# Optimization experiments

Hardware: AMD Instinct MI355X
Metric: run time of the kernel (lower is better)

Reference implementation:

```python
import jax, jax.numpy as jnp
import numpy as np

N_NODES = 100000   # n_all_trajs
N_EDGES = 640000
HIDDEN = 128
N_USERS = 1000


def gcn_conv(x, edge_index, edge_weight, W, b, num_nodes):
    """PyG GCNConv with add_self_loops=False, normalize=True.
    out[col] += (deg^-1/2[row] * w * deg^-1/2[col]) * (x @ W)[row]; then + b.
    deg is weighted in-degree at the target (col) nodes."""
    row, col = edge_index[0], edge_index[1]
    deg = jax.ops.segment_sum(edge_weight, col, num_segments=num_nodes)
    deg_inv_sqrt = jnp.where(deg > 0, jax.lax.rsqrt(jnp.maximum(deg, 1e-30)), 0.0)
    norm = deg_inv_sqrt[row] * edge_weight * deg_inv_sqrt[col]   # [E]
    h = x @ W                                                    # [N, H]
    msg = h[row] * norm[:, None]                                 # [E, H] gather+scale
    out = jax.ops.segment_sum(msg, col, num_segments=num_nodes)  # scatter-add
    return out + b


def setup_inputs() -> dict:
    key = jax.random.key(0)
    ks = jax.random.split(key, 9)
    edge_index = jax.random.randint(ks[0], (2, N_EDGES), 0, N_NODES, dtype=jnp.int64)
    edge_weight = jax.random.uniform(ks[1], (N_EDGES,), dtype=jnp.float32)
    emb = jax.random.normal(ks[2], (N_NODES, HIDDEN), dtype=jnp.float32) * 0.02
    W1 = jax.random.normal(ks[3], (HIDDEN, HIDDEN), dtype=jnp.float32) * 0.05
    b1 = jax.random.normal(ks[4], (HIDDEN,), dtype=jnp.float32) * 0.01
    W2 = jax.random.normal(ks[5], (HIDDEN, HIDDEN), dtype=jnp.float32) * 0.05
    b2 = jax.random.normal(ks[6], (HIDDEN,), dtype=jnp.float32) * 0.01
    Wp = jax.random.normal(ks[7], (HIDDEN, N_USERS), dtype=jnp.float32) * 0.05
    bp = jax.random.normal(ks[8], (N_USERS,), dtype=jnp.float32) * 0.01
    return {"edge_index": edge_index, "edge_weight": edge_weight, "emb": emb,
            "W1": W1, "b1": b1, "W2": W2, "b2": b2, "Wp": Wp, "bp": bp}


def reference(edge_index, edge_weight, emb, W1, b1, W2, b2, Wp, bp):
    h1 = gcn_conv(emb, edge_index, edge_weight, W1, b1, N_NODES)
    # dropout p=0.0 (inference) -> identity
    h2 = gcn_conv(h1, edge_index, edge_weight, W2, b2, N_NODES)
    predictions = h2 @ Wp + bp   # [N_NODES, N_USERS]
    return predictions
```

## Files before the change

kernel.cpp:

```cpp
#include <hip/hip_runtime.h>

#define N_NODES 100000
#define N_EDGES 640000
#define HIDDEN  128
#define N_USERS 1000
#define CAP     64

using u16 = unsigned short;
using u32 = unsigned int;

using short8  = __attribute__((ext_vector_type(8))) short;
using floatx4 = __attribute__((ext_vector_type(4))) float;

__device__ __forceinline__ u16 f2bf(float f) {
  u32 u = __float_as_uint(f);
  u32 r = u + 0x7FFFu + ((u >> 16) & 1u);
  return (u16)(r >> 16);
}
__device__ __forceinline__ u32 pack2bf(float a, float b) {
  return (u32)f2bf(a) | ((u32)f2bf(b) << 16);
}
__device__ __forceinline__ float bflo2f(u32 v) { return __uint_as_float(v << 16); }


__global__ __launch_bounds__(256)
void prep_kernel(const float* __restrict__ emb, u16* __restrict__ xb,
                 const int* __restrict__ ecol, const float* __restrict__ ew,
                 float* __restrict__ deg,
                 const float* __restrict__ W1, const float* __restrict__ b1,
                 const float* __restrict__ W2,
                 float* __restrict__ T1, float* __restrict__ t1) {
  int b = blockIdx.x;
  if (b < 6250) {
    int i = b * 256 + threadIdx.x;
    const float4* s4 = (const float4*)(emb + (size_t)i * 8);
    float4 lo = s4[0], hi = s4[1];
    uint4 o;
    o.x = pack2bf(lo.x, lo.y); o.y = pack2bf(lo.z, lo.w);
    o.z = pack2bf(hi.x, hi.y); o.w = pack2bf(hi.z, hi.w);
    ((uint4*)xb)[i] = o;
  } else if (b < 8750) {
    int i = (b - 6250) * 256 + threadIdx.x;
    atomicAdd(&deg[ecol[i]], ew[i]);
  } else {
    int idx = (b - 8750) * 256 + threadIdx.x;
    if (idx >= 129 * 128) return;
    int k = idx >> 7, c = idx & 127;
    const float* src = (k < 128) ? (W1 + (size_t)k * 128) : b1;
    float s = 0.f;
    for (int j = 0; j < 128; ++j) s += src[j] * W2[(size_t)j * 128 + c];
    if (k < 128) T1[(size_t)k * 128 + c] = s;
    else         t1[c] = s;
  }
}

__global__ __launch_bounds__(256)
void stage2_kernel(const int* __restrict__ erow, const int* __restrict__ ecol,
                   const float* __restrict__ ew, const float* __restrict__ deg,
                   int* __restrict__ counts, int2* __restrict__ pairs,
                   const float* __restrict__ T1, const float* __restrict__ t1,
                   const float* __restrict__ b2, const float* __restrict__ Wp,
                   const float* __restrict__ bp,
                   u16* __restrict__ WcT, float* __restrict__ u, float* __restrict__ v) {
  int b = blockIdx.x;
  if (b < 2500) {
    int i = b * 256 + threadIdx.x;
    int r = erow[i], c = ecol[i];
    float dr = deg[r], dc = deg[c];
    float nr = dr > 0.f ? rsqrtf(dr) : 0.f;
    float nc = dc > 0.f ? rsqrtf(dc) : 0.f;
    int pos = atomicAdd(&counts[c], 1);
    if (pos < CAP)
      pairs[((size_t)c << 6) + (size_t)pos] = make_int2(r, __float_as_int(nr * ew[i] * nc));
  } else if (b < 3012) {
    int idx = (b - 2500) * 256 + threadIdx.x;
    int c = idx >> 7, k = idx & 127;
    float s = 0.f;
    if (c < N_USERS)
      for (int l = 0; l < 128; ++l) s += T1[(size_t)k * 128 + l] * Wp[(size_t)l * N_USERS + c];
    WcT[idx] = f2bf(s);
  } else {
    int idx = (b - 3012) * 256 + threadIdx.x;
    if (idx >= 2 * N_USERS) return;
    if (idx < N_USERS) {
      float s = 0.f;
      for (int j = 0; j < 128; ++j) s += t1[j] * Wp[(size_t)j * N_USERS + idx];
      u[idx] = s;
    } else {
      int c = idx - N_USERS;
      float s = bp[c];
      for (int j = 0; j < 128; ++j) s += b2[j] * Wp[(size_t)j * N_USERS + c];
      v[c] = s;
    }
  }
}

template<bool S1OUT>
__global__ __launch_bounds__(256)
void agg_kernel(const u16* __restrict__ hb, const int* __restrict__ counts,
                const int2* __restrict__ pairs, float* __restrict__ s1,
                u16* __restrict__ out, int M) {
  int wid  = threadIdx.x >> 6;
  int lane = threadIdx.x & 63;
  int n = blockIdx.x * 4 + wid;
  if (n >= M) return;
  int cnt = counts[n];
  cnt = cnt < CAP ? cnt : CAP;
  int2 my = make_int2(0, 0);
  if (lane < cnt) my = pairs[((size_t)n << 6) + lane];
  int   sv = my.x;
  float wv = __int_as_float(my.y);
  const uint2* h8 = (const uint2*)hb;
  int half = lane >> 5, l5 = lane & 31;
  float a0 = 0.f, a1 = 0.f, a2 = 0.f, a3 = 0.f;
  int trips = (cnt + 1) >> 1;
  int t = 0;
  for (; t + 2 <= trips; t += 2) {
    int e0 = 2 * t + half, e1 = 2 * t + 2 + half;
    int   s0 = __shfl(sv, e0), s1_ = __shfl(sv, e1);
    float w0 = __shfl(wv, e0), w1  = __shfl(wv, e1);
    uint2 h0 = h8[((size_t)s0  << 5) + l5];
    uint2 h1 = h8[((size_t)s1_ << 5) + l5];
    a0 += w0 * bflo2f(h0.x & 0xFFFFu); a1 += w0 * __uint_as_float(h0.x & 0xFFFF0000u);
    a2 += w0 * bflo2f(h0.y & 0xFFFFu); a3 += w0 * __uint_as_float(h0.y & 0xFFFF0000u);
    a0 += w1 * bflo2f(h1.x & 0xFFFFu); a1 += w1 * __uint_as_float(h1.x & 0xFFFF0000u);
    a2 += w1 * bflo2f(h1.y & 0xFFFFu); a3 += w1 * __uint_as_float(h1.y & 0xFFFF0000u);
  }
  for (; t < trips; ++t) {
    int e = 2 * t + half;
    int   s = __shfl(sv, e);
    float w = __shfl(wv, e);
    uint2 h = h8[((size_t)s << 5) + l5];
    a0 += w * bflo2f(h.x & 0xFFFFu); a1 += w * __uint_as_float(h.x & 0xFFFF0000u);
    a2 += w * bflo2f(h.y & 0xFFFFu); a3 += w * __uint_as_float(h.y & 0xFFFF0000u);
  }
  a0 += __shfl_xor(a0, 32); a1 += __shfl_xor(a1, 32);
  a2 += __shfl_xor(a2, 32); a3 += __shfl_xor(a3, 32);
  if (S1OUT) {
    float tt = wv;
    for (int o = 32; o; o >>= 1) tt += __shfl_xor(tt, o);
    if (lane == 0) s1[n] = tt;
  }
  if (half == 0) {
    uint2 o;
    o.x = pack2bf(a0, a1);
    o.y = pack2bf(a2, a3);
    ((uint2*)out)[((size_t)n << 5) + l5] = o;
  }
}

__global__ __launch_bounds__(256, 2)
void gemm_final(const u16* __restrict__ A, const u16* __restrict__ BT,
                const float* __restrict__ s1, const float* __restrict__ u,
                const float* __restrict__ vv, float* __restrict__ outf, int M) {
  __shared__ u16 smem[2 * 128 * 128];
  u16* As = smem;
  u16* Bs = smem + 128 * 128;
  const int m0 = (blockIdx.x >> 3) * 128;
  const int n0 = (blockIdx.x & 7) * 128;
  const int tid = threadIdx.x;

  for (int i = 0; i < 8; ++i) {
    int chunk = tid + i * 256;
    int row = chunk >> 4;
    int c   = chunk & 15;
    int sw  = ((c ^ (row & 15)) << 3);
    int gr  = m0 + row;
    uint4 av = {0u, 0u, 0u, 0u};
    if (gr < M) av = *(const uint4*)(A + ((size_t)gr << 7) + (c << 3));
    *(uint4*)(&As[(row << 7) + sw]) = av;
    uint4 bv = *(const uint4*)(BT + ((size_t)(n0 + row) << 7) + (c << 3));
    *(uint4*)(&Bs[(row << 7) + sw]) = bv;
  }
  __syncthreads();

  const int wid  = tid >> 6, lane = tid & 63;
  const int wr = (wid >> 1) << 6;
  const int wc = (wid & 1) << 6;
  const int lm = lane & 15, quad = lane >> 4;

  floatx4 acc[4][4] = {};
  for (int ks = 0; ks < 4; ++ks) {
    int cks = ks * 4 + quad;
    int sw  = ((cks ^ lm) << 3);
    short8 a[4], b[4];
    for (int i = 0; i < 4; ++i)
      a[i] = *(const short8*)(&As[((wr + i * 16 + lm) << 7) + sw]);
    for (int j = 0; j < 4; ++j)
      b[j] = *(const short8*)(&Bs[((wc + j * 16 + lm) << 7) + sw]);
    for (int i = 0; i < 4; ++i)
      for (int j = 0; j < 4; ++j)
        acc[i][j] = __builtin_amdgcn_mfma_f32_16x16x32_bf16(a[i], b[j], acc[i][j], 0, 0, 0);
  }

  float uc[4], vc[4];
  for (int j = 0; j < 4; ++j) {
    int col = n0 + wc + j * 16 + lm;
    bool ok = col < N_USERS;
    uc[j] = ok ? u[col]  : 0.f;
    vc[j] = ok ? vv[col] : 0.f;
  }
  float sr[4][4];
  for (int i = 0; i < 4; ++i)
    for (int r = 0; r < 4; ++r) {
      int row = m0 + wr + i * 16 + quad * 4 + r;
      sr[i][r] = (row < M) ? s1[row] : 0.f;
    }

  __syncthreads();
  float* Os = (float*)smem;
  for (int i = 0; i < 4; ++i)
    for (int j = 0; j < 4; ++j)
      for (int r = 0; r < 4; ++r) {
        int lrow = wr + i * 16 + quad * 4 + r;
        int lcol = wc + j * 16 + lm;
        Os[(lrow << 7) + lcol] = acc[i][j][r] + sr[i][r] * uc[j] + vc[j];
      }
  __syncthreads();

  for (int k = 0; k < 16; ++k) {
    int f   = k * 256 + tid;
    int row = f >> 5;
    int c4  = f & 31;
    int gr  = m0 + row;
    int col = n0 + (c4 << 2);
    if (gr < M && col < N_USERS) {
      float4 val = *(const float4*)(Os + (row << 7) + (c4 << 2));
      *(float4*)(outf + (size_t)gr * N_USERS + col) = val;
    }
  }
}

extern "C" void kernel_launch(void* const* d_in, const int* in_sizes, int n_in,
                              void* d_out, int out_size, void* d_ws, size_t ws_size,
                              hipStream_t stream) {
  const int*   eidx = (const int*)d_in[0];
  const int*   erow = eidx;
  const int*   ecol = eidx + N_EDGES;
  const float* ew   = (const float*)d_in[1];
  const float* emb  = (const float*)d_in[2];
  const float* W1   = (const float*)d_in[3];
  const float* b1   = (const float*)d_in[4];
  const float* W2   = (const float*)d_in[5];
  const float* b2   = (const float*)d_in[6];
  const float* Wp   = (const float*)d_in[7];
  const float* bp   = (const float*)d_in[8];
  float* out = (float*)d_out;

  const int M = N_NODES;

  char* p = (char*)d_ws;
  float* deg    = (float*)p;  p += 400128;
  int*   counts = (int*)p;    p += 400128;
  float* s1     = (float*)p;  p += 400128;
  int2*  pairs  = (int2*)p;   p += (size_t)M * CAP * 8;
  u16*   Xb     = (u16*)p;    p += (size_t)M * 128 * 2;
  u16*   g      = (u16*)p;    p += (size_t)M * 128 * 2;
  float* T1     = (float*)p;  p += 128 * 128 * 4;
  float* t1     = (float*)p;  p += 512;
  u16*   WcT    = (u16*)p;    p += 1024 * 128 * 2;
  float* uvec   = (float*)p;  p += 4096;
  float* vvec   = (float*)p;  p += 4096;

  hipMemsetAsync(deg, 0, 400128 + 400128, stream);

  prep_kernel<<<8815, 256, 0, stream>>>(emb, Xb, ecol, ew, deg, W1, b1, W2, T1, t1);
  stage2_kernel<<<3020, 256, 0, stream>>>(erow, ecol, ew, deg, counts, pairs,
                                          T1, t1, b2, Wp, bp, WcT, uvec, vvec);

  agg_kernel<true ><<<(M + 3) / 4, 256, 0, stream>>>(Xb, counts, pairs, s1, g, M);
  agg_kernel<false><<<(M + 3) / 4, 256, 0, stream>>>(g,  counts, pairs, nullptr, Xb, M);

  const int mt = (M + 127) / 128;
  gemm_final<<<mt * 8, 256, 0, stream>>>(Xb, WcT, s1, uvec, vvec, out, M);
}
```

Baseline: 699.4 us.

## Halve gemm_final LDS, read B from global, and group blocks for L2 reuse

The final GEMM no longer stages the B (WcT) tile in shared memory. B fragments are read straight from global memory, where the small 1000x128 matrix should stay in cache. The output staging is split into two 64-row halves so a single 32KB LDS buffer is enough, and launch bounds rise to 4 blocks per CU. Block indices are remapped so that 8 consecutive M tiles share the same N tile, which is meant to improve L2 locality. The trade-offs are uncoalesced global B loads inside the MFMA loop, extra barriers, and a hardcoded grid of 98*64 blocks tied to N_NODES.

```diff
diff --git a/kernel.cpp b/kernel.cpp
--- a/kernel.cpp
+++ b/kernel.cpp
@@ -149,15 +149,17 @@
   }
 }
 
-__global__ __launch_bounds__(256, 2)
+__global__ __launch_bounds__(256, 4)
 void gemm_final(const u16* __restrict__ A, const u16* __restrict__ BT,
                 const float* __restrict__ s1, const float* __restrict__ u,
                 const float* __restrict__ vv, float* __restrict__ outf, int M) {
-  __shared__ u16 smem[2 * 128 * 128];
-  u16* As = smem;
-  u16* Bs = smem + 128 * 128;
-  const int m0 = (blockIdx.x >> 3) * 128;
-  const int n0 = (blockIdx.x & 7) * 128;
+  __shared__ u16 As[128 * 128];
+  const int bid = blockIdx.x;
+  const int g = bid >> 6, w = bid & 63;
+  const int mi = g * 8 + (w & 7);
+  if (mi >= (N_NODES + 127) / 128) return;
+  const int m0 = mi << 7;
+  const int n0 = (w >> 3) << 7;
   const int tid = threadIdx.x;
 
   for (int i = 0; i < 8; ++i) {
@@ -169,8 +171,6 @@
     uint4 av = {0u, 0u, 0u, 0u};
     if (gr < M) av = *(const uint4*)(A + ((size_t)gr << 7) + (c << 3));
     *(uint4*)(&As[(row << 7) + sw]) = av;
-    uint4 bv = *(const uint4*)(BT + ((size_t)(n0 + row) << 7) + (c << 3));
-    *(uint4*)(&Bs[(row << 7) + sw]) = bv;
   }
   __syncthreads();
 
@@ -187,7 +187,7 @@
     for (int i = 0; i < 4; ++i)
       a[i] = *(const short8*)(&As[((wr + i * 16 + lm) << 7) + sw]);
     for (int j = 0; j < 4; ++j)
-      b[j] = *(const short8*)(&Bs[((wc + j * 16 + lm) << 7) + sw]);
+      b[j] = *(const short8*)(BT + ((size_t)(n0 + wc + j * 16 + lm) << 7) + (cks << 3));
     for (int i = 0; i < 4; ++i)
       for (int j = 0; j < 4; ++j)
         acc[i][j] = __builtin_amdgcn_mfma_f32_16x16x32_bf16(a[i], b[j], acc[i][j], 0, 0, 0);
@@ -208,26 +208,30 @@
     }
 
   __syncthreads();
-  float* Os = (float*)smem;
-  for (int i = 0; i < 4; ++i)
-    for (int j = 0; j < 4; ++j)
-      for (int r = 0; r < 4; ++r) {
-        int lrow = wr + i * 16 + quad * 4 + r;
-        int lcol = wc + j * 16 + lm;
-        Os[(lrow << 7) + lcol] = acc[i][j][r] + sr[i][r] * uc[j] + vc[j];
+  float* Os = (float*)As;
+  for (int h = 0; h < 2; ++h) {
+    if ((wr >> 6) == h) {
+      for (int i = 0; i < 4; ++i)
+        for (int j = 0; j < 4; ++j)
+          for (int r = 0; r < 4; ++r) {
+            int lrow = i * 16 + quad * 4 + r;
+            int lcol = wc + j * 16 + lm;
+            Os[(lrow << 7) + lcol] = acc[i][j][r] + sr[i][r] * uc[j] + vc[j];
+          }
+    }
+    __syncthreads();
+    for (int k = 0; k < 8; ++k) {
+      int f   = k * 256 + tid;
+      int row = f >> 5;
+      int c4  = f & 31;
+      int gr  = m0 + h * 64 + row;
+      int col = n0 + (c4 << 2);
+      if (gr < M && col < N_USERS) {
+        float4 val = *(const float4*)(Os + (row << 7) + (c4 << 2));
+        *(float4*)(outf + (size_t)gr * N_USERS + col) = val;
       }
-  __syncthreads();
-
-  for (int k = 0; k < 16; ++k) {
-    int f   = k * 256 + tid;
-    int row = f >> 5;
-    int c4  = f & 31;
-    int gr  = m0 + row;
-    int col = n0 + (c4 << 2);
-    if (gr < M && col < N_USERS) {
-      float4 val = *(const float4*)(Os + (row << 7) + (c4 << 2));
-      *(float4*)(outf + (size_t)gr * N_USERS + col) = val;
-    }
+    }
+    __syncthreads();
   }
 }
 
@@ -271,6 +275,5 @@
   agg_kernel<true ><<<(M + 3) / 4, 256, 0, stream>>>(Xb, counts, pairs, s1, g, M);
   agg_kernel<false><<<(M + 3) / 4, 256, 0, stream>>>(g,  counts, pairs, nullptr, Xb, M);
 
-  const int mt = (M + 127) / 128;
-  gemm_final<<<mt * 8, 256, 0, stream>>>(Xb, WcT, s1, uvec, vvec, out, M);
-}
+  gemm_final<<<98 * 64, 256, 0, stream>>>(Xb, WcT, s1, uvec, vvec, out, M);
+}
```

New measurement: 668.6 us. 1.05x faster.
